# Optimization experiments

Measured on AMD Instinct MI355X. Metric: run time of the kernel, lower is better.

The kernel has to match this reference:

```python
import jax, jax.numpy as jnp
import numpy as np

MAX_GRAD = 200.0


@jax.custom_vjp
def sqrt_bound_derivative(x):
    return jnp.sqrt(x)


def _sqrt_bd_fwd(x):
    return jnp.sqrt(x), x


def _sqrt_bd_bwd(x, g):
    # derivative of sqrt clipped to MAX_GRAD: 0.5/sqrt(x) <= MAX_GRAD  <=>  x >= 1/(4*MAX_GRAD^2)
    x_clipped = jnp.maximum(x, 1.0 / (4.0 * MAX_GRAD * MAX_GRAD))
    return (g * 0.5 / jnp.sqrt(x_clipped),)


sqrt_bound_derivative.defvjp(_sqrt_bd_fwd, _sqrt_bd_bwd)


def linear_scan(a, x, h0):
    # h_t = a_t * h_{t-1} + x_t, diagonal recurrence over axis=1 (time).
    # Parallel form via associative scan on pairs (a, b): combine -> (a1*a2, a2*b1 + b2).
    def combine(c1, c2):
        a1, b1 = c1
        a2, b2 = c2
        return a1 * a2, a2 * b1 + b2

    a_cum, h = jax.lax.associative_scan(combine, (a, x), axis=1)
    # fold in initial state: h_t += (prod_{u<=t} a_u) * h0
    h = h + a_cum * h0[:, None, :]
    return h, h[:, -1]


def setup_inputs() -> dict:
    key = jax.random.key(0)
    ks = jax.random.split(key, 8)
    B, S, D_IN, D_HID, D_OUT = 8, 4096, 512, 1024, 512
    R_MIN, R_MAX = 0.9, 0.999

    x = jax.random.normal(ks[0], (B, S, D_IN), dtype=jnp.float32)
    h0 = jnp.zeros((B, D_HID), dtype=jnp.float32)

    # stable_init: a_logit = logit(U(r_min, r_max)) so that a = sigmoid(a_logit) in [r_min, r_max]
    u = jax.random.uniform(ks[1], (D_HID,), minval=R_MIN, maxval=R_MAX)
    a_logit = jnp.log(u) - jnp.log1p(-u)

    def dense_init(k, d_in, d_out):
        scale = 1.0 / np.sqrt(d_in)
        return jax.random.uniform(k, (d_in, d_out), minval=-scale, maxval=scale).astype(jnp.float32)

    W_dx = dense_init(ks[2], D_IN, D_OUT)
    b_dx = jnp.zeros((D_OUT,), dtype=jnp.float32)
    W_in = dense_init(ks[3], D_IN, D_HID)
    b_in = jnp.zeros((D_HID,), dtype=jnp.float32)
    W_out = dense_init(ks[4], D_HID, D_OUT)
    b_out = jnp.zeros((D_OUT,), dtype=jnp.float32)

    return {"x": x, "h0": h0, "a_logit": a_logit,
            "W_dx": W_dx, "b_dx": b_dx,
            "W_in": W_in, "b_in": b_in,
            "W_out": W_out, "b_out": b_out}


def reference(x, h0, a_logit, W_dx, b_dx, W_in, b_in, W_out, b_out):
    a = jax.nn.sigmoid(a_logit)                      # (d_hidden,)
    dx = jnp.einsum('bsi,io->bso', x, W_dx) + b_dx   # skip projection (b, s, d_out)
    u = jnp.einsum('bsi,ih->bsh', x, W_in) + b_in    # input projection (b, s, d_hidden)
    u = sqrt_bound_derivative(1.0 - a * a) * u       # input_norm gating
    a_b = jnp.broadcast_to(a, u.shape)
    h, h_last = linear_scan(a_b, u, h0)              # diagonal linear recurrence
    out = (dx + jnp.einsum('bsh,ho->bso', h, W_out) + b_out) / 2.0
    return out, h_last
```

## Files before the change

kernel.cpp:

```cpp
#include <hip/hip_runtime.h>

#define B_    8
#define S_    4096
#define DIN   512
#define DHID  1024
#define DOUT  512
#define M_    (B_*S_)
#define NCAT  (DHID + DOUT)
#define CHUNK 128
#define NCH   (S_/CHUNK)

typedef __bf16 bf16x8 __attribute__((ext_vector_type(8)));
typedef float  floatx4 __attribute__((ext_vector_type(4)));

__device__ __forceinline__ unsigned short f2bf(float f) {
  unsigned u = __builtin_bit_cast(unsigned, f);
  u = (u + 0x7FFFu + ((u >> 16) & 1u)) >> 16;
  return (unsigned short)u;
}
__device__ __forceinline__ float bf2f(unsigned short h) {
  unsigned u = ((unsigned)h) << 16;
  return __builtin_bit_cast(float, u);
}

__device__ __forceinline__ void gl_lds16(const unsigned short* g, unsigned short* l) {
  __builtin_amdgcn_global_load_lds((const __attribute__((address_space(1))) void*)g,
                                   (__attribute__((address_space(3))) void*)l, 16, 0, 0);
}

__global__ void prep_as(const float* __restrict__ logit, float* __restrict__ a_s) {
  int d = blockIdx.x * 256 + threadIdx.x;
  if (d < DHID) {
    float a = 1.f / (1.f + expf(-logit[d]));
    a_s[d] = a;
    a_s[DHID + d] = sqrtf(fmaxf(1.f - a * a, 0.f));
  }
}

__global__ void prep_x(const float* __restrict__ x, unsigned short* __restrict__ xb) {
  size_t i = (size_t)blockIdx.x * 256 + threadIdx.x;
  const float4* p = (const float4*)x;
  float4 v0 = p[i * 2];
  float4 v1 = p[i * 2 + 1];
  uint4 o;
  o.x = (unsigned)f2bf(v0.x) | ((unsigned)f2bf(v0.y) << 16);
  o.y = (unsigned)f2bf(v0.z) | ((unsigned)f2bf(v0.w) << 16);
  o.z = (unsigned)f2bf(v1.x) | ((unsigned)f2bf(v1.y) << 16);
  o.w = (unsigned)f2bf(v1.z) | ((unsigned)f2bf(v1.w) << 16);
  *(uint4*)&xb[i * 8] = o;
}

__global__ void prep_wcat(const float* __restrict__ Win, const float* __restrict__ Wdx,
                          unsigned short* __restrict__ wcat) {
  int idx = blockIdx.x * 256 + threadIdx.x;
  int n = idx >> 9, k = idx & 511;
  float v = (n < DHID) ? Win[(size_t)k * DHID + n] : Wdx[(size_t)k * DOUT + (n - DHID)];
  wcat[idx] = f2bf(v);
}

__global__ void prep_wout(const float* __restrict__ Wout, unsigned short* __restrict__ wt) {
  int idx = blockIdx.x * 256 + threadIdx.x;
  int n = idx >> 10, k = idx & 1023;
  wt[idx] = f2bf(Wout[(size_t)k * DOUT + n]);
}

template <int K, int MODE>
__global__ __launch_bounds__(256) void gemm_bt(
    const unsigned short* __restrict__ A,
    const unsigned short* __restrict__ Bt,
    const float* __restrict__ a_s,
    const float* __restrict__ bias0,
    const float* __restrict__ bias1,
    unsigned short* __restrict__ u_out,
    unsigned short* __restrict__ dx_buf,
    float* __restrict__ out)
{
  __shared__ __align__(16) unsigned char smem[32768];
  unsigned short* lA = (unsigned short*)smem;
  unsigned short* lB = (unsigned short*)(smem + 16384);
  float* stg = (float*)smem;

  const int tid = threadIdx.x;
  const int n0 = blockIdx.x * 128, m0 = blockIdx.y * 128;
  const int wid = tid >> 6, lane = tid & 63;
  const int wm = (wid >> 1) * 64, wn = (wid & 1) * 64;
  const int r16 = lane & 15, quad = lane >> 4;
  const int sw = r16 & 7;

  const int rsub = lane >> 3;
  const int gcol = ((lane & 7) ^ rsub) << 3;

  const unsigned short* Abase = A + (size_t)(m0 + (wid << 5) + rsub) * K + gcol;
  const unsigned short* Bbase = Bt + (size_t)(n0 + (wid << 5) + rsub) * K + gcol;
  unsigned short* lAw = lA + (wid << 5) * 64;
  unsigned short* lBw = lB + (wid << 5) * 64;

  floatx4 acc[4][4] = {};

  for (int k0 = 0; k0 < K; k0 += 64) {
#pragma unroll
    for (int i = 0; i < 4; ++i) {
      gl_lds16(Abase + (size_t)(i * 8) * K + k0, lAw + i * 8 * 64);
      gl_lds16(Bbase + (size_t)(i * 8) * K + k0, lBw + i * 8 * 64);
    }
    __syncthreads();
#pragma unroll
    for (int ks = 0; ks < 2; ++ks) {
      bf16x8 af[4], bfr[4];
#pragma unroll
      for (int i = 0; i < 4; ++i)
        af[i] = *(const bf16x8*)&lA[(wm + i * 16 + r16) * 64 + ((((ks << 2) | quad) ^ sw) << 3)];
#pragma unroll
      for (int j = 0; j < 4; ++j)
        bfr[j] = *(const bf16x8*)&lB[(wn + j * 16 + r16) * 64 + ((((ks << 2) | quad) ^ sw) << 3)];
#pragma unroll
      for (int i = 0; i < 4; ++i)
#pragma unroll
        for (int j = 0; j < 4; ++j)
          acc[i][j] = __builtin_amdgcn_mfma_f32_16x16x32_bf16(af[i], bfr[j], acc[i][j], 0, 0, 0);
    }
    __syncthreads();
  }

  const int row = tid >> 3;
  const int seg = tid & 7;
#pragma unroll
  for (int p = 0; p < 4; ++p) {
    __syncthreads();
    if ((wid >> 1) == (p >> 1)) {
      const int i0 = (p & 1) * 2;
#pragma unroll
      for (int ii = 0; ii < 2; ++ii) {
        const int i = i0 + ii;
        const int srow = i * 16 + quad * 4 - (p & 1) * 32;
#pragma unroll
        for (int j = 0; j < 4; ++j) {
          const int scol = wn + j * 16 + r16;
#pragma unroll
          for (int r = 0; r < 4; ++r)
            stg[(srow + r) * 132 + scol] = acc[i][j][r];
        }
      }
    }
    __syncthreads();
    const int gm = m0 + p * 32 + row;
    const int col0 = n0 + seg * 16;
    if (MODE == 0) {
      union { unsigned short s[16]; uint4 q[2]; } ub;
      if (n0 < DHID) {
#pragma unroll
        for (int u = 0; u < 4; ++u) {
          float4 v  = *(const float4*)&stg[row * 132 + seg * 16 + u * 4];
          float4 bi = *(const float4*)&bias0[col0 + u * 4];
          float4 sc = *(const float4*)&a_s[DHID + col0 + u * 4];
          ub.s[u * 4 + 0] = f2bf((v.x + bi.x) * sc.x);
          ub.s[u * 4 + 1] = f2bf((v.y + bi.y) * sc.y);
          ub.s[u * 4 + 2] = f2bf((v.z + bi.z) * sc.z);
          ub.s[u * 4 + 3] = f2bf((v.w + bi.w) * sc.w);
        }
        *(uint4*)&u_out[(size_t)gm * DHID + col0]     = ub.q[0];
        *(uint4*)&u_out[(size_t)gm * DHID + col0 + 8] = ub.q[1];
      } else {
        const int c2 = col0 - DHID;
#pragma unroll
        for (int u = 0; u < 4; ++u) {
          float4 v  = *(const float4*)&stg[row * 132 + seg * 16 + u * 4];
          float4 bd = *(const float4*)&bias1[c2 + u * 4];
          ub.s[u * 4 + 0] = f2bf(v.x + bd.x);
          ub.s[u * 4 + 1] = f2bf(v.y + bd.y);
          ub.s[u * 4 + 2] = f2bf(v.z + bd.z);
          ub.s[u * 4 + 3] = f2bf(v.w + bd.w);
        }
        *(uint4*)&dx_buf[(size_t)gm * DOUT + c2]     = ub.q[0];
        *(uint4*)&dx_buf[(size_t)gm * DOUT + c2 + 8] = ub.q[1];
      }
    } else {
#pragma unroll
      for (int u = 0; u < 4; ++u) {
        float4 v  = *(const float4*)&stg[row * 132 + seg * 16 + u * 4];
        float4 bo = *(const float4*)&bias0[col0 + u * 4];
        ushort4 dv = *(const ushort4*)&dx_buf[(size_t)gm * DOUT + col0 + u * 4];
        float4 o;
        o.x = (v.x + bo.x + bf2f(dv.x)) * 0.5f;
        o.y = (v.y + bo.y + bf2f(dv.y)) * 0.5f;
        o.z = (v.z + bo.z + bf2f(dv.z)) * 0.5f;
        o.w = (v.w + bo.w + bf2f(dv.w)) * 0.5f;
        *(float4*)&out[(size_t)gm * DOUT + col0 + u * 4] = o;
      }
    }
  }
}

__global__ __launch_bounds__(256) void scan1(const unsigned short* __restrict__ u,
                                             const float* __restrict__ a_s,
                                             float* __restrict__ carry) {
  int idx = blockIdx.x * 256 + threadIdx.x;
  int d = idx & (DHID - 1);
  int c = (idx >> 10) & (NCH - 1);
  int b = idx >> 15;
  float a = a_s[d];
  float h = 0.f;
  const unsigned short* up = u + ((size_t)(b * S_ + c * CHUNK)) * DHID + d;
#pragma unroll 4
  for (int t = 0; t < CHUNK; ++t)
    h = fmaf(a, h, bf2f(up[(size_t)t * DHID]));
  carry[((size_t)b * NCH + c) * DHID + d] = h;
}

__global__ __launch_bounds__(256) void scan_mid(const float* __restrict__ a_s,
                                                const float* __restrict__ h0,
                                                float* __restrict__ carry) {
  int idx = blockIdx.x * 256 + threadIdx.x;
  int d = idx & (DHID - 1);
  int b = idx >> 10;
  float a = a_s[d];
  float aL = a;
#pragma unroll
  for (int q = 0; q < 7; ++q) aL *= aL;
  float st = h0[(size_t)b * DHID + d];
#pragma unroll
  for (int c = 0; c < NCH; ++c) {
    float* p = &carry[((size_t)b * NCH + c) * DHID + d];
    float loc = *p;
    *p = st;
    st = fmaf(aL, st, loc);
  }
}

__global__ __launch_bounds__(256) void scan2(unsigned short* __restrict__ u,
                                             const float* __restrict__ a_s,
                                             const float* __restrict__ carry,
                                             float* __restrict__ h_last) {
  int idx = blockIdx.x * 256 + threadIdx.x;
  int d = idx & (DHID - 1);
  int c = (idx >> 10) & (NCH - 1);
  int b = idx >> 15;
  float a = a_s[d];
  float h = carry[((size_t)b * NCH + c) * DHID + d];
  unsigned short* up = u + ((size_t)(b * S_ + c * CHUNK)) * DHID + d;
#pragma unroll 4
  for (int t = 0; t < CHUNK; ++t) {
    h = fmaf(a, h, bf2f(up[(size_t)t * DHID]));
    up[(size_t)t * DHID] = f2bf(h);
  }
  if (c == NCH - 1) h_last[(size_t)b * DHID + d] = h;
}

extern "C" void kernel_launch(void* const* d_in, const int* in_sizes, int n_in,
                              void* d_out, int out_size, void* d_ws, size_t ws_size,
                              hipStream_t stream) {
  const float* x    = (const float*)d_in[0];
  const float* h0   = (const float*)d_in[1];
  const float* alog = (const float*)d_in[2];
  const float* Wdx  = (const float*)d_in[3];
  const float* bdx  = (const float*)d_in[4];
  const float* Win  = (const float*)d_in[5];
  const float* bin  = (const float*)d_in[6];
  const float* Wout = (const float*)d_in[7];
  const float* bout = (const float*)d_in[8];

  float* out    = (float*)d_out;
  float* h_last = out + (size_t)M_ * DOUT;

  char* ws = (char*)d_ws;
  unsigned short* xb    = (unsigned short*)(ws);
  unsigned short* ubuf  = (unsigned short*)(ws + 33554432ull);
  unsigned short* dxb   = (unsigned short*)(ws + 100663296ull);
  unsigned short* wcat  = (unsigned short*)(ws + 134217728ull);
  unsigned short* woutt = (unsigned short*)(ws + 135790592ull);
  float*          a_s   = (float*)(ws + 136839168ull);
  float*          carry = (float*)(ws + 136847360ull);

  prep_as  <<<4, 256, 0, stream>>>(alog, a_s);
  prep_x   <<<(M_ * DIN / 8) / 256, 256, 0, stream>>>(x, xb);
  prep_wcat<<<(NCAT * DIN) / 256, 256, 0, stream>>>(Win, Wdx, wcat);
  prep_wout<<<(DOUT * DHID) / 256, 256, 0, stream>>>(Wout, woutt);

  gemm_bt<DIN, 0><<<dim3(NCAT / 128, M_ / 128), 256, 0, stream>>>(
      xb, wcat, a_s, bin, bdx, ubuf, dxb, nullptr);

  scan1   <<<(B_ * NCH * DHID) / 256, 256, 0, stream>>>(ubuf, a_s, carry);
  scan_mid<<<(B_ * DHID) / 256, 256, 0, stream>>>(a_s, h0, carry);
  scan2   <<<(B_ * NCH * DHID) / 256, 256, 0, stream>>>(ubuf, a_s, carry, h_last);

  gemm_bt<DHID, 1><<<dim3(DOUT / 128, M_ / 128), 256, 0, stream>>>(
      ubuf, woutt, a_s, bout, nullptr, nullptr, dxb, out);
}
```

Measured before the change: 320.2 us.

## Vectorize chunked scan, shrink chunks, remap GEMM blocks for XCD locality

The scan kernels now have each thread handle 8 hidden channels with 8-byte loads and stores, and chunk length drops from 128 to 32. This gives more parallel chunks and wider memory accesses in place of strided 2-byte accesses. scan_mid now writes h_last directly, and the carry buffer is moved to reuse the xb region of the workspace. Both GEMMs remap the flat block index so that consecutive blocks landing on the same XCD share A-row tiles, aiming at better L2 reuse. The risks are a longer serial loop in scan_mid (128 chunks instead of 32) and a larger carry buffer.

```diff
diff --git a/kernel.cpp b/kernel.cpp
--- a/kernel.cpp
+++ b/kernel.cpp
@@ -7,8 +7,8 @@
 #define DOUT  512
 #define M_    (B_*S_)
 #define NCAT  (DHID + DOUT)
-#define CHUNK 128
-#define NCH   (S_/CHUNK)
+#define CH2   32
+#define NCH2  (S_/CH2)
 
 typedef __bf16 bf16x8 __attribute__((ext_vector_type(8)));
 typedef float  floatx4 __attribute__((ext_vector_type(4)));
@@ -64,7 +64,7 @@
   wt[idx] = f2bf(Wout[(size_t)k * DOUT + n]);
 }
 
-template <int K, int MODE>
+template <int K, int MODE, int NB>
 __global__ __launch_bounds__(256) void gemm_bt(
     const unsigned short* __restrict__ A,
     const unsigned short* __restrict__ Bt,
@@ -81,7 +81,12 @@
   float* stg = (float*)smem;
 
   const int tid = threadIdx.x;
-  const int n0 = blockIdx.x * 128, m0 = blockIdx.y * 128;
+  const int flat = blockIdx.y * gridDim.x + blockIdx.x;
+  const int xcd = flat & 7;
+  const int j = flat >> 3;
+  const int n0 = (j % NB) * 128;
+  const int m0 = ((j / NB) * 8 + xcd) * 128;
+
   const int wid = tid >> 6, lane = tid & 63;
   const int wm = (wid >> 1) * 64, wn = (wid & 1) * 64;
   const int r16 = lane & 15, quad = lane >> 4;
@@ -111,13 +116,13 @@
       for (int i = 0; i < 4; ++i)
         af[i] = *(const bf16x8*)&lA[(wm + i * 16 + r16) * 64 + ((((ks << 2) | quad) ^ sw) << 3)];
 #pragma unroll
-      for (int j = 0; j < 4; ++j)
-        bfr[j] = *(const bf16x8*)&lB[(wn + j * 16 + r16) * 64 + ((((ks << 2) | quad) ^ sw) << 3)];
+      for (int j2 = 0; j2 < 4; ++j2)
+        bfr[j2] = *(const bf16x8*)&lB[(wn + j2 * 16 + r16) * 64 + ((((ks << 2) | quad) ^ sw) << 3)];
 #pragma unroll
       for (int i = 0; i < 4; ++i)
 #pragma unroll
-        for (int j = 0; j < 4; ++j)
-          acc[i][j] = __builtin_amdgcn_mfma_f32_16x16x32_bf16(af[i], bfr[j], acc[i][j], 0, 0, 0);
+        for (int j2 = 0; j2 < 4; ++j2)
+          acc[i][j2] = __builtin_amdgcn_mfma_f32_16x16x32_bf16(af[i], bfr[j2], acc[i][j2], 0, 0, 0);
     }
     __syncthreads();
   }
@@ -134,11 +139,11 @@
         const int i = i0 + ii;
         const int srow = i * 16 + quad * 4 - (p & 1) * 32;
 #pragma unroll
-        for (int j = 0; j < 4; ++j) {
-          const int scol = wn + j * 16 + r16;
+        for (int j2 = 0; j2 < 4; ++j2) {
+          const int scol = wn + j2 * 16 + r16;
 #pragma unroll
           for (int r = 0; r < 4; ++r)
-            stg[(srow + r) * 132 + scol] = acc[i][j][r];
+            stg[(srow + r) * 132 + scol] = acc[i][j2][r];
         }
       }
     }
@@ -195,55 +200,80 @@
                                              const float* __restrict__ a_s,
                                              float* __restrict__ carry) {
   int idx = blockIdx.x * 256 + threadIdx.x;
-  int d = idx & (DHID - 1);
-  int c = (idx >> 10) & (NCH - 1);
-  int b = idx >> 15;
-  float a = a_s[d];
-  float h = 0.f;
-  const unsigned short* up = u + ((size_t)(b * S_ + c * CHUNK)) * DHID + d;
+  int d8 = (idx & 127) * 8;
+  int c  = (idx >> 7) & (NCH2 - 1);
+  int b  = idx >> 14;
+  float4 a0 = *(const float4*)&a_s[d8];
+  float4 a1 = *(const float4*)&a_s[d8 + 4];
+  float h0_ = 0.f, h1 = 0.f, h2 = 0.f, h3 = 0.f, h4 = 0.f, h5 = 0.f, h6 = 0.f, h7 = 0.f;
+  const unsigned short* up = u + ((size_t)(b * S_ + c * CH2)) * DHID + d8;
 #pragma unroll 4
-  for (int t = 0; t < CHUNK; ++t)
-    h = fmaf(a, h, bf2f(up[(size_t)t * DHID]));
-  carry[((size_t)b * NCH + c) * DHID + d] = h;
+  for (int t = 0; t < CH2; ++t) {
+    ushort4 q0 = *(const ushort4*)up;
+    ushort4 q1 = *(const ushort4*)(up + 4);
+    h0_ = fmaf(a0.x, h0_, bf2f(q0.x)); h1 = fmaf(a0.y, h1, bf2f(q0.y));
+    h2  = fmaf(a0.z, h2,  bf2f(q0.z)); h3 = fmaf(a0.w, h3, bf2f(q0.w));
+    h4  = fmaf(a1.x, h4,  bf2f(q1.x)); h5 = fmaf(a1.y, h5, bf2f(q1.y));
+    h6  = fmaf(a1.z, h6,  bf2f(q1.z)); h7 = fmaf(a1.w, h7, bf2f(q1.w));
+    up += DHID;
+  }
+  float* cp = &carry[((size_t)(b * NCH2 + c)) * DHID + d8];
+  float4 o0 = {h0_, h1, h2, h3}, o1 = {h4, h5, h6, h7};
+  *(float4*)cp = o0;
+  *(float4*)(cp + 4) = o1;
 }
 
 __global__ __launch_bounds__(256) void scan_mid(const float* __restrict__ a_s,
                                                 const float* __restrict__ h0,
-                                                float* __restrict__ carry) {
+                                                float* __restrict__ carry,
+                                                float* __restrict__ h_last) {
   int idx = blockIdx.x * 256 + threadIdx.x;
   int d = idx & (DHID - 1);
   int b = idx >> 10;
   float a = a_s[d];
   float aL = a;
 #pragma unroll
-  for (int q = 0; q < 7; ++q) aL *= aL;
+  for (int q = 0; q < 5; ++q) aL *= aL;
   float st = h0[(size_t)b * DHID + d];
-#pragma unroll
-  for (int c = 0; c < NCH; ++c) {
-    float* p = &carry[((size_t)b * NCH + c) * DHID + d];
+  for (int c = 0; c < NCH2; ++c) {
+    float* p = &carry[((size_t)b * NCH2 + c) * DHID + d];
     float loc = *p;
     *p = st;
     st = fmaf(aL, st, loc);
   }
+  h_last[(size_t)b * DHID + d] = st;
 }
 
 __global__ __launch_bounds__(256) void scan2(unsigned short* __restrict__ u,
                                              const float* __restrict__ a_s,
-                                             const float* __restrict__ carry,
-                                             float* __restrict__ h_last) {
-  int idx = blockIdx.x * 256 + threadIdx.x;
-  int d = idx & (DHID - 1);
-  int c = (idx >> 10) & (NCH - 1);
-  int b = idx >> 15;
-  float a = a_s[d];
-  float h = carry[((size_t)b * NCH + c) * DHID + d];
-  unsigned short* up = u + ((size_t)(b * S_ + c * CHUNK)) * DHID + d;
+                                             const float* __restrict__ carry) {
+  int idx = blockIdx.x * 256 + threadIdx.x;
+  int d8 = (idx & 127) * 8;
+  int c  = (idx >> 7) & (NCH2 - 1);
+  int b  = idx >> 14;
+  float4 a0 = *(const float4*)&a_s[d8];
+  float4 a1 = *(const float4*)&a_s[d8 + 4];
+  const float* cp = &carry[((size_t)(b * NCH2 + c)) * DHID + d8];
+  float4 e0 = *(const float4*)cp;
+  float4 e1 = *(const float4*)(cp + 4);
+  float h0_ = e0.x, h1 = e0.y, h2 = e0.z, h3 = e0.w;
+  float h4 = e1.x, h5 = e1.y, h6 = e1.z, h7 = e1.w;
+  unsigned short* up = u + ((size_t)(b * S_ + c * CH2)) * DHID + d8;
 #pragma unroll 4
-  for (int t = 0; t < CHUNK; ++t) {
-    h = fmaf(a, h, bf2f(up[(size_t)t * DHID]));
-    up[(size_t)t * DHID] = f2bf(h);
-  }
-  if (c == NCH - 1) h_last[(size_t)b * DHID + d] = h;
+  for (int t = 0; t < CH2; ++t) {
+    ushort4 q0 = *(const ushort4*)up;
+    ushort4 q1 = *(const ushort4*)(up + 4);
+    h0_ = fmaf(a0.x, h0_, bf2f(q0.x)); h1 = fmaf(a0.y, h1, bf2f(q0.y));
+    h2  = fmaf(a0.z, h2,  bf2f(q0.z)); h3 = fmaf(a0.w, h3, bf2f(q0.w));
+    h4  = fmaf(a1.x, h4,  bf2f(q1.x)); h5 = fmaf(a1.y, h5, bf2f(q1.y));
+    h6  = fmaf(a1.z, h6,  bf2f(q1.z)); h7 = fmaf(a1.w, h7, bf2f(q1.w));
+    ushort4 w0, w1;
+    w0.x = f2bf(h0_); w0.y = f2bf(h1); w0.z = f2bf(h2); w0.w = f2bf(h3);
+    w1.x = f2bf(h4);  w1.y = f2bf(h5); w1.z = f2bf(h6); w1.w = f2bf(h7);
+    *(ushort4*)up = w0;
+    *(ushort4*)(up + 4) = w1;
+    up += DHID;
+  }
 }
 
 extern "C" void kernel_launch(void* const* d_in, const int* in_sizes, int n_in,
@@ -269,20 +299,20 @@
   unsigned short* wcat  = (unsigned short*)(ws + 134217728ull);
   unsigned short* woutt = (unsigned short*)(ws + 135790592ull);
   float*          a_s   = (float*)(ws + 136839168ull);
-  float*          carry = (float*)(ws + 136847360ull);
+  float*          carry = (float*)(ws);
 
   prep_as  <<<4, 256, 0, stream>>>(alog, a_s);
   prep_x   <<<(M_ * DIN / 8) / 256, 256, 0, stream>>>(x, xb);
   prep_wcat<<<(NCAT * DIN) / 256, 256, 0, stream>>>(Win, Wdx, wcat);
   prep_wout<<<(DOUT * DHID) / 256, 256, 0, stream>>>(Wout, woutt);
 
-  gemm_bt<DIN, 0><<<dim3(NCAT / 128, M_ / 128), 256, 0, stream>>>(
+  gemm_bt<DIN, 0, 12><<<dim3(NCAT / 128, M_ / 128), 256, 0, stream>>>(
       xb, wcat, a_s, bin, bdx, ubuf, dxb, nullptr);
 
-  scan1   <<<(B_ * NCH * DHID) / 256, 256, 0, stream>>>(ubuf, a_s, carry);
-  scan_mid<<<(B_ * DHID) / 256, 256, 0, stream>>>(a_s, h0, carry);
-  scan2   <<<(B_ * NCH * DHID) / 256, 256, 0, stream>>>(ubuf, a_s, carry, h_last);
-
-  gemm_bt<DHID, 1><<<dim3(DOUT / 128, M_ / 128), 256, 0, stream>>>(
+  scan1   <<<(B_ * NCH2 * (DHID / 8)) / 256, 256, 0, stream>>>(ubuf, a_s, carry);
+  scan_mid<<<(B_ * DHID) / 256, 256, 0, stream>>>(a_s, h0, carry, h_last);
+  scan2   <<<(B_ * NCH2 * (DHID / 8)) / 256, 256, 0, stream>>>(ubuf, a_s, carry);
+
+  gemm_bt<DHID, 1, 4><<<dim3(DOUT / 128, M_ / 128), 256, 0, stream>>>(
       ubuf, woutt, a_s, bout, nullptr, nullptr, dxb, out);
 }
```

New measurement: 303.4 us. 5.2% less time.
